# Kernel optimization log

Hardware: AMD Instinct MI355X
Metric: run time of the kernel (lower is better)

## Reference

```python
import jax, jax.numpy as jnp
import numpy as np

NEG_SLOPE = 0.2
EPS = 1e-16


def _segment_softmax(alpha, idx, num_segments):
    # alpha: [E, H], idx: [E] destination node ids
    m = jax.ops.segment_max(alpha, idx, num_segments=num_segments)
    alpha = jnp.exp(alpha - m[idx])
    s = jax.ops.segment_sum(alpha, idx, num_segments=num_segments)
    return alpha / (s[idx] + EPS)


def _gat_conv(x, src, dst, W, a_src, a_dst, b, concat):
    # x: [N, F_in], W: [F_in, H*C], a_src/a_dst: [H, C], b: [H*C] or [C]
    N = x.shape[0]
    H, C = a_src.shape
    h = (x @ W).reshape(N, H, C)                      # [N, H, C]
    alpha_s = jnp.einsum('nhc,hc->nh', h, a_src)      # [N, H]
    alpha_d = jnp.einsum('nhc,hc->nh', h, a_dst)      # [N, H]
    # PyG GATConv adds self-loops by default
    loop = jnp.arange(N, dtype=src.dtype)
    src2 = jnp.concatenate([src, loop])
    dst2 = jnp.concatenate([dst, loop])
    e = jax.nn.leaky_relu(alpha_s[src2] + alpha_d[dst2], NEG_SLOPE)  # [E+N, H]
    att = _segment_softmax(e, dst2, N)                # [E+N, H]
    msg = h[src2] * att[..., None]                    # [E+N, H, C]
    out = jax.ops.segment_sum(msg, dst2, num_segments=N)  # [N, H, C]
    out = out.reshape(N, H * C) if concat else out.mean(axis=1)
    return out + b


def setup_inputs() -> dict:
    key = jax.random.key(0)
    ks = jax.random.split(key, 16)
    N, E, F_in, H, C, C_out = 50000, 800000, 128, 4, 32, 64
    sc = lambda f: 1.0 / np.sqrt(f)
    inp = {
        'x': jax.random.normal(ks[0], (N, F_in), dtype=jnp.float32),
        'edge_index': jax.random.randint(ks[1], (2, E), 0, N, dtype=jnp.int64),
        'W0': jax.random.normal(ks[2], (F_in, H * C), dtype=jnp.float32) * sc(F_in),
        'a_src0': jax.random.normal(ks[3], (H, C), dtype=jnp.float32) * sc(C),
        'a_dst0': jax.random.normal(ks[4], (H, C), dtype=jnp.float32) * sc(C),
        'b0': jnp.zeros((H * C,), dtype=jnp.float32),
        'W1': jax.random.normal(ks[5], (H * C, H * C), dtype=jnp.float32) * sc(H * C),
        'a_src1': jax.random.normal(ks[6], (H, C), dtype=jnp.float32) * sc(C),
        'a_dst1': jax.random.normal(ks[7], (H, C), dtype=jnp.float32) * sc(C),
        'b1': jnp.zeros((H * C,), dtype=jnp.float32),
        'W2': jax.random.normal(ks[8], (H * C, H * C_out), dtype=jnp.float32) * sc(H * C),
        'a_src2': jax.random.normal(ks[9], (H, C_out), dtype=jnp.float32) * sc(C_out),
        'a_dst2': jax.random.normal(ks[10], (H, C_out), dtype=jnp.float32) * sc(C_out),
        'b2': jnp.zeros((C_out,), dtype=jnp.float32),
    }
    return inp


def reference(x, edge_index, W0, a_src0, a_dst0, b0, W1, a_src1, a_dst1, b1,
              W2, a_src2, a_dst2, b2):
    src, dst = edge_index[0], edge_index[1]
    # layer 0 (concat=True) -> relu (dropout is identity in eval mode)
    h = _gat_conv(x, src, dst, W0, a_src0, a_dst0, b0, concat=True)
    h = jax.nn.relu(h)
    # layer 1 (concat=True) -> relu
    h = _gat_conv(h, src, dst, W1, a_src1, a_dst1, b1, concat=True)
    h = jax.nn.relu(h)
    # layer 2 (concat=False, head mean)
    out = _gat_conv(h, src, dst, W2, a_src2, a_dst2, b2, concat=False)
    return out
```

## Files before the change

### kernel.cpp

```cpp
#include <hip/hip_runtime.h>
#include <hip/hip_fp16.h>
#include <math.h>

#define NEG_SLOPE 0.2f
#define GAT_EPS 1e-16f

__device__ __forceinline__ float lrelu(float x) { return x > 0.f ? x : NEG_SLOPE * x; }

__device__ __forceinline__ void fma_row4(float4& a, float w, uint2 u) {
    const float2 f0 = __half22float2(*(const __half2*)&u.x);
    const float2 f1 = __half22float2(*(const __half2*)&u.y);
    a.x += w * f0.x; a.y += w * f0.y;
    a.z += w * f1.x; a.w += w * f1.y;
}

__device__ __forceinline__ void fma_row2(float2& a, float w, unsigned u) {
    const float2 f = __half22float2(*(const __half2*)&u);
    a.x += w * f.x; a.y += w * f.y;
}

__global__ __launch_bounds__(256) void gemm_tiled(
    const float* __restrict__ A, const float* __restrict__ B,
    float* __restrict__ C, __half* __restrict__ C16, int M, int K, int Ncol)
{
    __shared__ float As[16][65];
    __shared__ float Bs[16][64];

    const int t  = threadIdx.x;
    const int bm = blockIdx.x * 64;
    const int bn = blockIdx.y * 64;
    const int tx = t & 15;
    const int ty = t >> 4;

    float acc[4][4] = {};

    for (int k0 = 0; k0 < K; k0 += 16) {
        {
            const int r  = t >> 2;
            const int kq = (t & 3) * 4;
            float4 v = make_float4(0.f, 0.f, 0.f, 0.f);
            const int row = bm + r;
            if (row < M) v = *(const float4*)(A + (size_t)row * K + k0 + kq);
            As[kq + 0][r] = v.x; As[kq + 1][r] = v.y;
            As[kq + 2][r] = v.z; As[kq + 3][r] = v.w;
        }
        {
            const int k  = t >> 4;
            const int nq = (t & 15) * 4;
            float4 v = *(const float4*)(B + (size_t)(k0 + k) * Ncol + bn + nq);
            *(float4*)(&Bs[k][nq]) = v;
        }
        __syncthreads();

        #pragma unroll
        for (int k = 0; k < 16; ++k) {
            float a[4], b[4];
            #pragma unroll
            for (int i = 0; i < 4; ++i) a[i] = As[k][ty * 4 + i];
            #pragma unroll
            for (int j = 0; j < 4; ++j) b[j] = Bs[k][tx * 4 + j];
            #pragma unroll
            for (int i = 0; i < 4; ++i)
                #pragma unroll
                for (int j = 0; j < 4; ++j)
                    acc[i][j] += a[i] * b[j];
        }
        __syncthreads();
    }

    #pragma unroll
    for (int i = 0; i < 4; ++i) {
        const int row = bm + ty * 4 + i;
        if (row < M) {
            #pragma unroll
            for (int j = 0; j < 4; ++j) {
                const float v = acc[i][j];
                const size_t idx = (size_t)row * Ncol + bn + tx * 4 + j;
                if (C)   C[idx]   = v;
                if (C16) C16[idx] = __float2half_rn(v);
            }
        }
    }
}

__global__ __launch_bounds__(256) void alpha_kernel(
    const float* __restrict__ h, const float* __restrict__ a_src,
    const float* __restrict__ a_dst, float* __restrict__ as_,
    float* __restrict__ ad_, int N, int HC, int C)
{
    const int i = blockIdx.x * blockDim.x + threadIdx.x;
    if (i >= N * 4) return;
    const int n  = i >> 2;
    const int hh = i & 3;
    const float* hp  = h + (size_t)n * HC + hh * C;
    const float* asp = a_src + hh * C;
    const float* adp = a_dst + hh * C;
    float s1 = 0.f, s2 = 0.f;
    for (int c = 0; c < C; c += 4) {
        const float4 v = *(const float4*)(hp + c);
        const float4 A = *(const float4*)(asp + c);
        const float4 D = *(const float4*)(adp + c);
        s1 += v.x * A.x + v.y * A.y + v.z * A.z + v.w * A.w;
        s2 += v.x * D.x + v.y * D.y + v.z * D.z + v.w * D.w;
    }
    as_[i] = s1;
    ad_[i] = s2;
}

__global__ __launch_bounds__(256) void alpha16_kernel(
    const __half* __restrict__ h, const float* __restrict__ a_src,
    const float* __restrict__ a_dst, float* __restrict__ as_,
    float* __restrict__ ad_, int N, int HC, int C)
{
    const int i = blockIdx.x * blockDim.x + threadIdx.x;
    if (i >= N * 4) return;
    const int n  = i >> 2;
    const int hh = i & 3;
    const __half* hp = h + (size_t)n * HC + hh * C;
    const float* asp = a_src + hh * C;
    const float* adp = a_dst + hh * C;
    float s1 = 0.f, s2 = 0.f;
    for (int c = 0; c < C; c += 2) {
        const float2 f = __half22float2(*(const __half2*)(hp + c));
        s1 += f.x * asp[c] + f.y * asp[c + 1];
        s2 += f.x * adp[c] + f.y * adp[c + 1];
    }
    as_[i] = s1;
    ad_[i] = s2;
}

__global__ __launch_bounds__(256) void zero_kernel(int* __restrict__ p, int n)
{
    const int i = blockIdx.x * 256 + threadIdx.x;
    if (i < n) p[i] = 0;
}

__global__ __launch_bounds__(256) void count_kernel(
    const int* __restrict__ ei, int* __restrict__ deg, int E)
{
    const int e = blockIdx.x * 256 + threadIdx.x;
    if (e < E) atomicAdd(&deg[ei[E + e]], 1);
}

__global__ __launch_bounds__(256) void scan_part_kernel(
    const int* __restrict__ deg, int* __restrict__ bsum, int N)
{
    __shared__ int red[256];
    const int b = blockIdx.x;
    const int t = threadIdx.x;
    const int base = b * 1024 + t * 4;
    int s = 0;
    #pragma unroll
    for (int i = 0; i < 4; ++i) {
        const int idx = base + i;
        if (idx < N) s += deg[idx];
    }
    red[t] = s;
    __syncthreads();
    for (int off = 128; off; off >>= 1) {
        if (t < off) red[t] += red[t + off];
        __syncthreads();
    }
    if (t == 0) bsum[b] = red[0];
}

__global__ __launch_bounds__(256) void scan_top_kernel(
    int* __restrict__ bsum, int B)
{
    __shared__ int sh[256];
    const int t = threadIdx.x;
    const int v = (t < B) ? bsum[t] : 0;
    sh[t] = v;
    __syncthreads();
    for (int off = 1; off < 256; off <<= 1) {
        const int u = (t >= off) ? sh[t - off] : 0;
        __syncthreads();
        sh[t] += u;
        __syncthreads();
    }
    if (t < B) bsum[t] = sh[t] - v;
}

__global__ __launch_bounds__(256) void scan_out_kernel(
    const int* __restrict__ deg, const int* __restrict__ bsum,
    int* __restrict__ rp, int N)
{
    __shared__ int red[256];
    const int b = blockIdx.x;
    const int t = threadIdx.x;
    const int base = b * 1024 + t * 4;
    int v[4]; int s = 0;
    #pragma unroll
    for (int i = 0; i < 4; ++i) {
        const int idx = base + i;
        v[i] = (idx < N) ? deg[idx] : 0;
        s += v[i];
    }
    red[t] = s;
    __syncthreads();
    for (int off = 1; off < 256; off <<= 1) {
        const int u = (t >= off) ? red[t - off] : 0;
        __syncthreads();
        red[t] += u;
        __syncthreads();
    }
    int run = bsum[b] + ((t > 0) ? red[t - 1] : 0);
    if (b == 0 && t == 0) rp[0] = 0;
    #pragma unroll
    for (int i = 0; i < 4; ++i) {
        const int idx = base + i;
        if (idx < N) { rp[idx + 1] = run; run += v[i]; }
    }
}

__global__ __launch_bounds__(256) void scatter_kernel(
    const int* __restrict__ ei, int* __restrict__ rp, int* __restrict__ col, int E)
{
    const int e = blockIdx.x * 256 + threadIdx.x;
    if (e < E) {
        const int dn  = ei[E + e];
        const int pos = atomicAdd(&rp[dn + 1], 1);
        col[pos] = ei[e];
    }
}

__global__ __launch_bounds__(256) void agg32_kernel(
    const __half* __restrict__ h16, const float* __restrict__ as_,
    const float* __restrict__ ad_, const int* __restrict__ rp,
    const int* __restrict__ col, const float* __restrict__ bias,
    float* __restrict__ out, int N)
{
    __shared__ float2 ared[4][64];
    __shared__ float  sred[4][4];
    const int n    = blockIdx.x;
    const int t    = threadIdx.x;
    const int w    = t >> 6;
    const int lane = t & 63;
    const int head = lane >> 4;
    const int start = rp[n];
    const int d     = rp[n + 1] - start;
    const float adn = ad_[n * 4 + head];

    float ss = 0.f;
    float2 a0 = {0.f, 0.f}, a1 = {0.f, 0.f}, a2 = {0.f, 0.f}, a3 = {0.f, 0.f};

    int e = w;
    for (; e + 12 < d; e += 16) {
        const int s0 = col[start + e];
        const int s1 = col[start + e + 4];
        const int s2 = col[start + e + 8];
        const int s3 = col[start + e + 12];
        const float w0 = __expf(lrelu(as_[s0 * 4 + head] + adn));
        const float w1 = __expf(lrelu(as_[s1 * 4 + head] + adn));
        const float w2 = __expf(lrelu(as_[s2 * 4 + head] + adn));
        const float w3 = __expf(lrelu(as_[s3 * 4 + head] + adn));
        const unsigned u0 = *(const unsigned*)(h16 + (size_t)s0 * 128 + 2 * lane);
        const unsigned u1 = *(const unsigned*)(h16 + (size_t)s1 * 128 + 2 * lane);
        const unsigned u2 = *(const unsigned*)(h16 + (size_t)s2 * 128 + 2 * lane);
        const unsigned u3 = *(const unsigned*)(h16 + (size_t)s3 * 128 + 2 * lane);
        ss += (w0 + w1) + (w2 + w3);
        fma_row2(a0, w0, u0);
        fma_row2(a1, w1, u1);
        fma_row2(a2, w2, u2);
        fma_row2(a3, w3, u3);
    }
    for (; e < d; e += 4) {
        const int s = col[start + e];
        const float wt = __expf(lrelu(as_[s * 4 + head] + adn));
        const unsigned u = *(const unsigned*)(h16 + (size_t)s * 128 + 2 * lane);
        ss += wt;
        fma_row2(a0, wt, u);
    }
    if (w == 0) {
        const float wt = __expf(lrelu(as_[n * 4 + head] + adn));
        const unsigned u = *(const unsigned*)(h16 + (size_t)n * 128 + 2 * lane);
        ss += wt;
        fma_row2(a0, wt, u);
    }

    float2 at;
    at.x = (a0.x + a1.x) + (a2.x + a3.x);
    at.y = (a0.y + a1.y) + (a2.y + a3.y);
    ared[w][lane] = at;
    if ((lane & 15) == 0) sred[w][head] = ss;
    __syncthreads();

    if (t < 128) {
        const int ch = t;
        const int hh = ch >> 5;
        const float ssum = sred[0][hh] + sred[1][hh] + sred[2][hh] + sred[3][hh];
        const float* ap0 = (const float*)ared[0];
        const float* ap1 = (const float*)ared[1];
        const float* ap2 = (const float*)ared[2];
        const float* ap3 = (const float*)ared[3];
        const float acc = (ap0[ch] + ap1[ch]) + (ap2[ch] + ap3[ch]);
        const float r = acc / (ssum + GAT_EPS) + bias[ch];
        out[(size_t)n * 128 + ch] = fmaxf(r, 0.f);
    }
}

__global__ __launch_bounds__(256) void agg64_mean_kernel(
    const __half* __restrict__ h16, const float* __restrict__ as_,
    const float* __restrict__ ad_, const int* __restrict__ rp,
    const int* __restrict__ col, const float* __restrict__ b2,
    float* __restrict__ out, int N)
{
    __shared__ float4 ared[4][64];
    __shared__ float  sred[4][4];
    const int n    = blockIdx.x;
    const int t    = threadIdx.x;
    const int w    = t >> 6;
    const int lane = t & 63;
    const int head = lane >> 4;
    const int start = rp[n];
    const int d     = rp[n + 1] - start;
    const float adn = ad_[n * 4 + head];

    float ss = 0.f;
    float4 a0 = {0,0,0,0}, a1 = {0,0,0,0}, a2 = {0,0,0,0}, a3 = {0,0,0,0};

    int e = w;
    for (; e + 12 < d; e += 16) {
        const int s0 = col[start + e];
        const int s1 = col[start + e + 4];
        const int s2 = col[start + e + 8];
        const int s3 = col[start + e + 12];
        const float w0 = __expf(lrelu(as_[s0 * 4 + head] + adn));
        const float w1 = __expf(lrelu(as_[s1 * 4 + head] + adn));
        const float w2 = __expf(lrelu(as_[s2 * 4 + head] + adn));
        const float w3 = __expf(lrelu(as_[s3 * 4 + head] + adn));
        const uint2 u0 = *(const uint2*)(h16 + (size_t)s0 * 256 + 4 * lane);
        const uint2 u1 = *(const uint2*)(h16 + (size_t)s1 * 256 + 4 * lane);
        const uint2 u2 = *(const uint2*)(h16 + (size_t)s2 * 256 + 4 * lane);
        const uint2 u3 = *(const uint2*)(h16 + (size_t)s3 * 256 + 4 * lane);
        ss += (w0 + w1) + (w2 + w3);
        fma_row4(a0, w0, u0);
        fma_row4(a1, w1, u1);
        fma_row4(a2, w2, u2);
        fma_row4(a3, w3, u3);
    }
    for (; e < d; e += 4) {
        const int s = col[start + e];
        const float wt = __expf(lrelu(as_[s * 4 + head] + adn));
        const uint2 u = *(const uint2*)(h16 + (size_t)s * 256 + 4 * lane);
        ss += wt;
        fma_row4(a0, wt, u);
    }
    if (w == 0) {
        const float wt = __expf(lrelu(as_[n * 4 + head] + adn));
        const uint2 u = *(const uint2*)(h16 + (size_t)n * 256 + 4 * lane);
        ss += wt;
        fma_row4(a0, wt, u);
    }

    float4 at;
    at.x = (a0.x + a1.x) + (a2.x + a3.x);
    at.y = (a0.y + a1.y) + (a2.y + a3.y);
    at.z = (a0.z + a1.z) + (a2.z + a3.z);
    at.w = (a0.w + a1.w) + (a2.w + a3.w);
    ared[w][lane] = at;
    if ((lane & 15) == 0) sred[w][head] = ss;
    __syncthreads();

    if (t < 64) {
        float is[4];
        #pragma unroll
        for (int h = 0; h < 4; ++h)
            is[h] = 1.f / (sred[0][h] + sred[1][h] + sred[2][h] + sred[3][h] + GAT_EPS);
        const float* ap0 = (const float*)ared[0];
        const float* ap1 = (const float*)ared[1];
        const float* ap2 = (const float*)ared[2];
        const float* ap3 = (const float*)ared[3];
        float o = 0.f;
        #pragma unroll
        for (int h = 0; h < 4; ++h) {
            const int ch = h * 64 + t;
            o += ((ap0[ch] + ap1[ch]) + (ap2[ch] + ap3[ch])) * is[h];
        }
        out[(size_t)n * 64 + t] = 0.25f * o + b2[t];
    }
}

extern "C" void kernel_launch(void* const* d_in, const int* in_sizes, int n_in,
                              void* d_out, int out_size, void* d_ws, size_t ws_size,
                              hipStream_t stream)
{
    const float* x   = (const float*)d_in[0];
    const int*   ei  = (const int*)d_in[1];
    const float* W0  = (const float*)d_in[2];
    const float* aS0 = (const float*)d_in[3];
    const float* aD0 = (const float*)d_in[4];
    const float* b0  = (const float*)d_in[5];
    const float* W1  = (const float*)d_in[6];
    const float* aS1 = (const float*)d_in[7];
    const float* aD1 = (const float*)d_in[8];
    const float* b1  = (const float*)d_in[9];
    const float* W2  = (const float*)d_in[10];
    const float* aS2 = (const float*)d_in[11];
    const float* aD2 = (const float*)d_in[12];
    const float* b2  = (const float*)d_in[13];

    const int N = in_sizes[0] / 128;
    const int E = in_sizes[1] / 2;

    float* ws     = (float*)d_ws;
    float* bufA   = ws;
    __half* h16a  = (__half*)(ws + (size_t)N * 128);
    __half* h2_16 = (__half*)ws;
    float* o_buf  = ws + (size_t)N * 256;
    float* as_buf = ws + (size_t)N * 384;
    float* ad_buf = ws + (size_t)N * 388;
    int*   rp     = (int*)(ws + (size_t)N * 392);
    int*   col    = (int*)(ws + (size_t)N * 394);
    int*   deg    = (int*)(ws + (size_t)N * 394) + E;
    int*   bsum   = deg + N;

    const int TB  = 256;
    const int gN  = (N + TB - 1) / TB;
    const int gE  = (E + TB - 1) / TB;
    const int gNH = (N * 4 + TB - 1) / TB;
    const int gS  = (N + 1023) / 1024;

    zero_kernel<<<gN, TB, 0, stream>>>(deg, N);
    count_kernel<<<gE, TB, 0, stream>>>(ei, deg, E);
    scan_part_kernel<<<gS, TB, 0, stream>>>(deg, bsum, N);
    scan_top_kernel<<<1, TB, 0, stream>>>(bsum, gS);
    scan_out_kernel<<<gS, TB, 0, stream>>>(deg, bsum, rp, N);
    scatter_kernel<<<gE, TB, 0, stream>>>(ei, rp, col, E);

    {
        dim3 g((N + 63) / 64, 2);
        gemm_tiled<<<g, TB, 0, stream>>>(x, W0, bufA, h16a, N, 128, 128);
        alpha_kernel<<<gNH, TB, 0, stream>>>(bufA, aS0, aD0, as_buf, ad_buf, N, 128, 32);
        agg32_kernel<<<N, TB, 0, stream>>>(h16a, as_buf, ad_buf, rp, col, b0, o_buf, N);
    }
    {
        dim3 g((N + 63) / 64, 2);
        gemm_tiled<<<g, TB, 0, stream>>>(o_buf, W1, bufA, h16a, N, 128, 128);
        alpha_kernel<<<gNH, TB, 0, stream>>>(bufA, aS1, aD1, as_buf, ad_buf, N, 128, 32);
        agg32_kernel<<<N, TB, 0, stream>>>(h16a, as_buf, ad_buf, rp, col, b1, o_buf, N);
    }
    {
        dim3 g((N + 63) / 64, 4);
        gemm_tiled<<<g, TB, 0, stream>>>(o_buf, W2, nullptr, h2_16, N, 128, 256);
        alpha16_kernel<<<gNH, TB, 0, stream>>>(h2_16, aS2, aD2, as_buf, ad_buf, N, 256, 64);
        agg64_mean_kernel<<<N, TB, 0, stream>>>(h2_16, as_buf, ad_buf, rp, col, b2, (float*)d_out, N);
    }
}
```

Measured before the change: 607.6 us.

## Use MFMA fp16 GEMM for layer 2 and one-wave-per-node aggregation

Replaces the fp32 tiled GEMM for the last layer with an MFMA 16x16x32 f16 kernel. It reads a half-precision copy of the layer-1 output plus a pre-packed fp16 W2 that is laid out for direct fragment loads. The aggregation kernels now give each node a single wavefront instead of a 4-wave block. This removes the shared-memory reduction and __syncthreads, and the final head mean is done with cross-lane shuffles. Costs: fp16 rounding of the GEMM inputs, an extra packing kernel, and less edge parallelism per node.

```diff
diff --git a/kernel.cpp b/kernel.cpp
--- a/kernel.cpp
+++ b/kernel.cpp
@@ -4,6 +4,9 @@
 
 #define NEG_SLOPE 0.2f
 #define GAT_EPS 1e-16f
+
+typedef _Float16 f16x8 __attribute__((ext_vector_type(8)));
+typedef float    f32x4 __attribute__((ext_vector_type(4)));
 
 __device__ __forceinline__ float lrelu(float x) { return x > 0.f ? x : NEG_SLOPE * x; }
 
@@ -79,6 +82,58 @@
                 if (C)   C[idx]   = v;
                 if (C16) C16[idx] = __float2half_rn(v);
             }
+        }
+    }
+}
+
+__global__ __launch_bounds__(256) void pack_w2_kernel(
+    const float* __restrict__ W2, __half* __restrict__ Wpk)
+{
+    const int idx = blockIdx.x * 256 + threadIdx.x;
+    const int k = idx >> 8;
+    const int c = idx & 255;
+    const int ks = k >> 5;
+    const int g  = (k >> 3) & 3;
+    const int i  = k & 7;
+    Wpk[((size_t)(ks * 256 + c) * 4 + g) * 8 + i] = __float2half_rn(W2[idx]);
+}
+
+__global__ __launch_bounds__(256) void gemm2_mfma(
+    const __half* __restrict__ A16, const __half* __restrict__ Wpk,
+    __half* __restrict__ C16, int M)
+{
+    const int t  = threadIdx.x;
+    const int w  = t >> 6;
+    const int l  = t & 63;
+    const int bm = blockIdx.x * 64;
+    const int bn = blockIdx.y * 64;
+    const int row = bm + w * 16 + (l & 15);
+    const int kg  = l >> 4;
+    const bool rok = row < M;
+
+    f32x4 acc[4] = {};
+
+    #pragma unroll
+    for (int ks = 0; ks < 4; ++ks) {
+        f16x8 a = {};
+        if (rok)
+            a = *(const f16x8*)(A16 + (size_t)row * 128 + ks * 32 + kg * 8);
+        #pragma unroll
+        for (int f = 0; f < 4; ++f) {
+            const f16x8 b = *(const f16x8*)(Wpk +
+                ((size_t)(ks * 256 + bn + f * 16 + (l & 15)) * 4 + kg) * 8);
+            acc[f] = __builtin_amdgcn_mfma_f32_16x16x32_f16(a, b, acc[f], 0, 0, 0);
+        }
+    }
+
+    const int orow = bm + w * 16 + (l >> 4) * 4;
+    #pragma unroll
+    for (int f = 0; f < 4; ++f) {
+        const int ccol = bn + f * 16 + (l & 15);
+        #pragma unroll
+        for (int r = 0; r < 4; ++r) {
+            if (orow + r < M)
+                C16[(size_t)(orow + r) * 256 + ccol] = __float2half_rn(acc[f][r]);
         }
     }
 }
@@ -228,14 +283,11 @@
     const __half* __restrict__ h16, const float* __restrict__ as_,
     const float* __restrict__ ad_, const int* __restrict__ rp,
     const int* __restrict__ col, const float* __restrict__ bias,
-    float* __restrict__ out, int N)
-{
-    __shared__ float2 ared[4][64];
-    __shared__ float  sred[4][4];
-    const int n    = blockIdx.x;
-    const int t    = threadIdx.x;
-    const int w    = t >> 6;
-    const int lane = t & 63;
+    float* __restrict__ out, __half* __restrict__ out16, int N)
+{
+    const int n = blockIdx.x * 4 + (threadIdx.x >> 6);
+    if (n >= N) return;
+    const int lane = threadIdx.x & 63;
     const int head = lane >> 4;
     const int start = rp[n];
     const int d     = rp[n + 1] - start;
@@ -244,12 +296,12 @@
     float ss = 0.f;
     float2 a0 = {0.f, 0.f}, a1 = {0.f, 0.f}, a2 = {0.f, 0.f}, a3 = {0.f, 0.f};
 
-    int e = w;
-    for (; e + 12 < d; e += 16) {
-        const int s0 = col[start + e];
-        const int s1 = col[start + e + 4];
-        const int s2 = col[start + e + 8];
-        const int s3 = col[start + e + 12];
+    int e = 0;
+    for (; e + 4 <= d; e += 4) {
+        const int s0 = col[start + e + 0];
+        const int s1 = col[start + e + 1];
+        const int s2 = col[start + e + 2];
+        const int s3 = col[start + e + 3];
         const float w0 = __expf(lrelu(as_[s0 * 4 + head] + adn));
         const float w1 = __expf(lrelu(as_[s1 * 4 + head] + adn));
         const float w2 = __expf(lrelu(as_[s2 * 4 + head] + adn));
@@ -264,39 +316,30 @@
         fma_row2(a2, w2, u2);
         fma_row2(a3, w3, u3);
     }
-    for (; e < d; e += 4) {
+    for (; e < d; ++e) {
         const int s = col[start + e];
         const float wt = __expf(lrelu(as_[s * 4 + head] + adn));
         const unsigned u = *(const unsigned*)(h16 + (size_t)s * 128 + 2 * lane);
         ss += wt;
         fma_row2(a0, wt, u);
     }
-    if (w == 0) {
+    {
         const float wt = __expf(lrelu(as_[n * 4 + head] + adn));
         const unsigned u = *(const unsigned*)(h16 + (size_t)n * 128 + 2 * lane);
         ss += wt;
         fma_row2(a0, wt, u);
     }
 
-    float2 at;
-    at.x = (a0.x + a1.x) + (a2.x + a3.x);
-    at.y = (a0.y + a1.y) + (a2.y + a3.y);
-    ared[w][lane] = at;
-    if ((lane & 15) == 0) sred[w][head] = ss;
-    __syncthreads();
-
-    if (t < 128) {
-        const int ch = t;
-        const int hh = ch >> 5;
-        const float ssum = sred[0][hh] + sred[1][hh] + sred[2][hh] + sred[3][hh];
-        const float* ap0 = (const float*)ared[0];
-        const float* ap1 = (const float*)ared[1];
-        const float* ap2 = (const float*)ared[2];
-        const float* ap3 = (const float*)ared[3];
-        const float acc = (ap0[ch] + ap1[ch]) + (ap2[ch] + ap3[ch]);
-        const float r = acc / (ssum + GAT_EPS) + bias[ch];
-        out[(size_t)n * 128 + ch] = fmaxf(r, 0.f);
-    }
+    float2 v;
+    v.x = (a0.x + a1.x) + (a2.x + a3.x);
+    v.y = (a0.y + a1.y) + (a2.y + a3.y);
+    const float inv = 1.f / (ss + GAT_EPS);
+    const float2 bb = *(const float2*)(bias + 2 * lane);
+    v.x = fmaxf(v.x * inv + bb.x, 0.f);
+    v.y = fmaxf(v.y * inv + bb.y, 0.f);
+    *(float2*)(out + (size_t)n * 128 + 2 * lane) = v;
+    if (out16)
+        *(__half2*)(out16 + (size_t)n * 128 + 2 * lane) = __floats2half2_rn(v.x, v.y);
 }
 
 __global__ __launch_bounds__(256) void agg64_mean_kernel(
@@ -305,12 +348,9 @@
     const int* __restrict__ col, const float* __restrict__ b2,
     float* __restrict__ out, int N)
 {
-    __shared__ float4 ared[4][64];
-    __shared__ float  sred[4][4];
-    const int n    = blockIdx.x;
-    const int t    = threadIdx.x;
-    const int w    = t >> 6;
-    const int lane = t & 63;
+    const int n = blockIdx.x * 4 + (threadIdx.x >> 6);
+    if (n >= N) return;
+    const int lane = threadIdx.x & 63;
     const int head = lane >> 4;
     const int start = rp[n];
     const int d     = rp[n + 1] - start;
@@ -319,12 +359,12 @@
     float ss = 0.f;
     float4 a0 = {0,0,0,0}, a1 = {0,0,0,0}, a2 = {0,0,0,0}, a3 = {0,0,0,0};
 
-    int e = w;
-    for (; e + 12 < d; e += 16) {
-        const int s0 = col[start + e];
-        const int s1 = col[start + e + 4];
-        const int s2 = col[start + e + 8];
-        const int s3 = col[start + e + 12];
+    int e = 0;
+    for (; e + 4 <= d; e += 4) {
+        const int s0 = col[start + e + 0];
+        const int s1 = col[start + e + 1];
+        const int s2 = col[start + e + 2];
+        const int s3 = col[start + e + 3];
         const float w0 = __expf(lrelu(as_[s0 * 4 + head] + adn));
         const float w1 = __expf(lrelu(as_[s1 * 4 + head] + adn));
         const float w2 = __expf(lrelu(as_[s2 * 4 + head] + adn));
@@ -339,45 +379,39 @@
         fma_row4(a2, w2, u2);
         fma_row4(a3, w3, u3);
     }
-    for (; e < d; e += 4) {
+    for (; e < d; ++e) {
         const int s = col[start + e];
         const float wt = __expf(lrelu(as_[s * 4 + head] + adn));
         const uint2 u = *(const uint2*)(h16 + (size_t)s * 256 + 4 * lane);
         ss += wt;
         fma_row4(a0, wt, u);
     }
-    if (w == 0) {
+    {
         const float wt = __expf(lrelu(as_[n * 4 + head] + adn));
         const uint2 u = *(const uint2*)(h16 + (size_t)n * 256 + 4 * lane);
         ss += wt;
         fma_row4(a0, wt, u);
     }
 
-    float4 at;
-    at.x = (a0.x + a1.x) + (a2.x + a3.x);
-    at.y = (a0.y + a1.y) + (a2.y + a3.y);
-    at.z = (a0.z + a1.z) + (a2.z + a3.z);
-    at.w = (a0.w + a1.w) + (a2.w + a3.w);
-    ared[w][lane] = at;
-    if ((lane & 15) == 0) sred[w][head] = ss;
-    __syncthreads();
-
-    if (t < 64) {
-        float is[4];
-        #pragma unroll
-        for (int h = 0; h < 4; ++h)
-            is[h] = 1.f / (sred[0][h] + sred[1][h] + sred[2][h] + sred[3][h] + GAT_EPS);
-        const float* ap0 = (const float*)ared[0];
-        const float* ap1 = (const float*)ared[1];
-        const float* ap2 = (const float*)ared[2];
-        const float* ap3 = (const float*)ared[3];
-        float o = 0.f;
-        #pragma unroll
-        for (int h = 0; h < 4; ++h) {
-            const int ch = h * 64 + t;
-            o += ((ap0[ch] + ap1[ch]) + (ap2[ch] + ap3[ch])) * is[h];
-        }
-        out[(size_t)n * 64 + t] = 0.25f * o + b2[t];
+    const float inv = 1.f / (ss + GAT_EPS);
+    float vx = ((a0.x + a1.x) + (a2.x + a3.x)) * inv;
+    float vy = ((a0.y + a1.y) + (a2.y + a3.y)) * inv;
+    float vz = ((a0.z + a1.z) + (a2.z + a3.z)) * inv;
+    float vw = ((a0.w + a1.w) + (a2.w + a3.w)) * inv;
+
+    vx += __shfl_xor(vx, 16); vx += __shfl_xor(vx, 32);
+    vy += __shfl_xor(vy, 16); vy += __shfl_xor(vy, 32);
+    vz += __shfl_xor(vz, 16); vz += __shfl_xor(vz, 32);
+    vw += __shfl_xor(vw, 16); vw += __shfl_xor(vw, 32);
+
+    if (lane < 16) {
+        const float4 bb = *(const float4*)(b2 + 4 * lane);
+        float4 o;
+        o.x = 0.25f * vx + bb.x;
+        o.y = 0.25f * vy + bb.y;
+        o.z = 0.25f * vz + bb.z;
+        o.w = 0.25f * vw + bb.w;
+        *(float4*)(out + (size_t)n * 64 + 4 * lane) = o;
     }
 }
 
@@ -406,6 +440,7 @@
     float* ws     = (float*)d_ws;
     float* bufA   = ws;
     __half* h16a  = (__half*)(ws + (size_t)N * 128);
+    __half* o16   = (__half*)(ws + (size_t)N * 192);
     __half* h2_16 = (__half*)ws;
     float* o_buf  = ws + (size_t)N * 256;
     float* as_buf = ws + (size_t)N * 384;
@@ -414,15 +449,18 @@
     int*   col    = (int*)(ws + (size_t)N * 394);
     int*   deg    = (int*)(ws + (size_t)N * 394) + E;
     int*   bsum   = deg + N;
+    __half* Wpk   = (__half*)(bsum + 256);
 
     const int TB  = 256;
     const int gN  = (N + TB - 1) / TB;
     const int gE  = (E + TB - 1) / TB;
     const int gNH = (N * 4 + TB - 1) / TB;
     const int gS  = (N + 1023) / 1024;
+    const int gA  = (N + 3) / 4;
 
     zero_kernel<<<gN, TB, 0, stream>>>(deg, N);
     count_kernel<<<gE, TB, 0, stream>>>(ei, deg, E);
+    pack_w2_kernel<<<128, TB, 0, stream>>>(W2, Wpk);
     scan_part_kernel<<<gS, TB, 0, stream>>>(deg, bsum, N);
     scan_top_kernel<<<1, TB, 0, stream>>>(bsum, gS);
     scan_out_kernel<<<gS, TB, 0, stream>>>(deg, bsum, rp, N);
@@ -432,18 +470,18 @@
         dim3 g((N + 63) / 64, 2);
         gemm_tiled<<<g, TB, 0, stream>>>(x, W0, bufA, h16a, N, 128, 128);
         alpha_kernel<<<gNH, TB, 0, stream>>>(bufA, aS0, aD0, as_buf, ad_buf, N, 128, 32);
-        agg32_kernel<<<N, TB, 0, stream>>>(h16a, as_buf, ad_buf, rp, col, b0, o_buf, N);
+        agg32_kernel<<<gA, TB, 0, stream>>>(h16a, as_buf, ad_buf, rp, col, b0, o_buf, nullptr, N);
     }
     {
         dim3 g((N + 63) / 64, 2);
         gemm_tiled<<<g, TB, 0, stream>>>(o_buf, W1, bufA, h16a, N, 128, 128);
         alpha_kernel<<<gNH, TB, 0, stream>>>(bufA, aS1, aD1, as_buf, ad_buf, N, 128, 32);
-        agg32_kernel<<<N, TB, 0, stream>>>(h16a, as_buf, ad_buf, rp, col, b1, o_buf, N);
+        agg32_kernel<<<gA, TB, 0, stream>>>(h16a, as_buf, ad_buf, rp, col, b1, o_buf, o16, N);
     }
     {
         dim3 g((N + 63) / 64, 4);
-        gemm_tiled<<<g, TB, 0, stream>>>(o_buf, W2, nullptr, h2_16, N, 128, 256);
+        gemm2_mfma<<<g, TB, 0, stream>>>(o16, Wpk, h2_16, N);
         alpha16_kernel<<<gNH, TB, 0, stream>>>(h2_16, aS2, aD2, as_buf, ad_buf, N, 256, 64);
-        agg64_mean_kernel<<<N, TB, 0, stream>>>(h2_16, as_buf, ad_buf, rp, col, b2, (float*)d_out, N);
-    }
-}
+        agg64_mean_kernel<<<gA, TB, 0, stream>>>(h2_16, as_buf, ad_buf, rp, col, b2, (float*)d_out, N);
+    }
+}
```

After: 517.6 us. 14.8% less time.
